# Kernel tuning notes

Measured on AMD Instinct MI355X. Metric: run time of the kernel, lower is better.

The kernel has to match this reference:

```python
import jax, jax.numpy as jnp
import numpy as np

B, T, V, H, F = 128, 20, 10000, 512, 49


def _uniform(key, shape, fan):
    s = 1.0 / np.sqrt(fan)
    return jax.random.uniform(key, shape, jnp.float32, -s, s)


def setup_inputs() -> dict:
    key = jax.random.key(0)
    ks = jax.random.split(key, 16)
    return {
        "caption_inputs": jax.random.randint(ks[0], (B, T), 0, V),
        "global_features": jax.random.normal(ks[1], (B, H), jnp.float32),
        "area_features": jax.random.normal(ks[2], (B, H, F), jnp.float32),
        "h0": jnp.zeros((B, H), jnp.float32),
        "c0": jnp.zeros((B, H), jnp.float32),
        # learned params
        "embedding": jax.random.normal(ks[3], (V, H), jnp.float32),
        "W_ih": _uniform(ks[4], (2 * H, 4 * H), H),   # LSTMCell input weights (x @ W_ih)
        "W_hh": _uniform(ks[5], (H, 4 * H), H),
        "b_ih": _uniform(ks[6], (4 * H,), H),
        "b_hh": _uniform(ks[7], (4 * H,), H),
        "Wv": _uniform(ks[8], (H, H), H),             # attention comp_visual
        "Wh": _uniform(ks[9], (H, H), H),             # attention comp_hidden
        "wo": _uniform(ks[10], (H,), H),              # attention output_layer
        "W_out": _uniform(ks[11], (2 * H, V), 2 * H), # decoder output layer
        "b_out": _uniform(ks[12], (V,), 2 * H),
    }


def reference(caption_inputs, global_features, area_features, h0, c0,
              embedding, W_ih, W_hh, b_ih, b_hh, Wv, Wh, wo, W_out, b_out):
    # Precompute attention visual projection (time-invariant): [B,F,H]
    feat = jnp.swapaxes(area_features, 1, 2)          # [B,F,H]
    Vproj = jnp.einsum('bfh,hk->bfk', feat, Wv)       # [B,F,H]
    bias = b_ih + b_hh

    def step(carry, tok):
        h, c = carry
        emb = embedding[tok]                           # [B,H]
        x = jnp.concatenate([emb, global_features], axis=1)   # [B,2H]
        gates = x @ W_ih + h @ W_hh + bias             # [B,4H]
        i, f, g, o = jnp.split(gates, 4, axis=1)
        c = jax.nn.sigmoid(f) * c + jax.nn.sigmoid(i) * jnp.tanh(g)
        h = jax.nn.sigmoid(o) * jnp.tanh(c)
        # spatial attention over F locations
        z = jnp.tanh(Vproj + (h @ Wh)[:, None, :])     # [B,F,H]
        scores = jnp.einsum('bfh,h->bf', z, wo)        # [B,F]
        alpha = jax.nn.softmax(scores, axis=1)
        attended = jnp.einsum('bhf,bf->bh', area_features, alpha)  # [B,H]
        out = jnp.concatenate([h, attended], axis=1) @ W_out + b_out  # [B,V]
        return (h, c), out

    (_, _), outs = jax.lax.scan(step, (h0, c0), caption_inputs.T)  # [T,B,V]
    return jnp.swapaxes(outs, 0, 1)                    # [B,T,V]
```

## Files before the change

### kernel.cpp

```cpp
#include <hip/hip_runtime.h>

#define B_ 128
#define T_ 20
#define V_ 10000
#define H_ 512
#define F_ 49
#define NBLK_ 128

typedef unsigned short u16;
typedef __attribute__((ext_vector_type(8))) short short8;
typedef __attribute__((ext_vector_type(4))) float floatx4;

#define GLOBAL_AS __attribute__((address_space(1)))
#define LDS_AS    __attribute__((address_space(3)))

__device__ inline void load_lds16(const void* g, void* l) {
    __builtin_amdgcn_global_load_lds((const GLOBAL_AS void*)g, (LDS_AS void*)l, 16, 0, 0);
}

__device__ inline u16 f2b(float v) {
    unsigned u = __builtin_bit_cast(unsigned, v);
    unsigned rounding = 0x7FFFu + ((u >> 16) & 1u);
    return (u16)((u + rounding) >> 16);
}
__device__ inline float b2f(u16 h) {
    unsigned u = ((unsigned)h) << 16;
    return __builtin_bit_cast(float, u);
}
__device__ inline float fast_tanh(float x) {
    return 1.f - 2.f / (__expf(2.f * x) + 1.f);
}
__device__ inline float sigm(float x) { return 1.f / (1.f + __expf(-x)); }

__device__ __forceinline__ void tr32(const float* __restrict__ src, u16* __restrict__ dst,
                                     int K, int N, int bx, int by, int tx, int ty,
                                     float (*tl)[33]) {
    int n0 = bx * 32, k0 = by * 32;
    #pragma unroll
    for (int i = 0; i < 32; i += 8) {
        int k = k0 + ty + i, n = n0 + tx;
        tl[ty + i][tx] = (k < K && n < N) ? src[(size_t)k * N + n] : 0.f;
    }
    __syncthreads();
    #pragma unroll
    for (int i = 0; i < 32; i += 8) {
        int n = n0 + ty + i, k = k0 + tx;
        if (n < N && k < K) dst[(size_t)n * K + k] = f2b(tl[tx][ty + i]);
    }
}

__global__ __launch_bounds__(256) void preamble(
        const float* __restrict__ W_ih, const float* __restrict__ W_hh,
        const float* __restrict__ Wv, const float* __restrict__ Wh,
        const float* __restrict__ W_out, const int* __restrict__ cap,
        const float* __restrict__ emb, const float* __restrict__ gf,
        const float* __restrict__ area, const float* __restrict__ h0,
        u16* __restrict__ WihT, u16* __restrict__ WhhT, u16* __restrict__ WvT,
        u16* __restrict__ WhT, u16* __restrict__ WoutT, u16* __restrict__ X,
        u16* __restrict__ feat, u16* __restrict__ Hall, int* __restrict__ bar) {
    __shared__ float tl[32][33];
    const int bid = blockIdx.x, tid = threadIdx.x;
    const int tx = tid & 31, ty = tid >> 5;

    if (bid < 2048) {
        int r = bid;                 tr32(W_ih, WihT, 1024, 2048, r % 64, r / 64, tx, ty, tl);
    } else if (bid < 3072) {
        int r = bid - 2048;          tr32(W_hh, WhhT, 512, 2048, r % 64, r / 64, tx, ty, tl);
    } else if (bid < 3328) {
        int r = bid - 3072;          tr32(Wv, WvT, 512, 512, r % 16, r / 16, tx, ty, tl);
    } else if (bid < 3584) {
        int r = bid - 3328;          tr32(Wh, WhT, 512, 512, r % 16, r / 16, tx, ty, tl);
    } else if (bid < 13600) {
        int r = bid - 3584;          tr32(W_out, WoutT, 1024, 10000, r % 313, r / 313, tx, ty, tl);
    } else if (bid < 16160) {
        int r = bid - 13600;
        int t = r / B_, b = r % B_;
        int tok = cap[b * T_ + t];
        for (int col = tid; col < 2 * H_; col += 256) {
            float v = (col < H_) ? emb[(size_t)tok * H_ + col] : gf[(size_t)b * H_ + (col - H_)];
            X[(size_t)r * (2 * H_) + col] = f2b(v);
        }
    } else if (bid < 20256) {
        int r = bid - 16160;
        int b = r >> 5, t32 = r & 31;
        int fx = t32 & 1, hy = t32 >> 1;
        tr32(area + (size_t)b * H_ * F_, feat + (size_t)b * F_ * H_,
             H_, F_, fx, hy, tx, ty, tl);
    } else {
        int r = bid - 20256;
        int i = r * 256 + tid;
        Hall[i] = f2b(h0[i]);
        if (r == 0) bar[tid] = 0;
    }
}

__device__ inline void grid_sync_mg(int* base, int ep) {
    __syncthreads();
    if (threadIdx.x == 0) {
        int old = __hip_atomic_fetch_add(&base[0], 1, __ATOMIC_ACQ_REL, __HIP_MEMORY_SCOPE_AGENT);
        if (old == ep * 32 - 1)
            __hip_atomic_store(&base[32], ep, __ATOMIC_RELEASE, __HIP_MEMORY_SCOPE_AGENT);
        while (__hip_atomic_load(&base[32], __ATOMIC_RELAXED, __HIP_MEMORY_SCOPE_AGENT) < ep)
            __builtin_amdgcn_s_sleep(2);
        (void)__hip_atomic_load(&base[32], __ATOMIC_ACQUIRE, __HIP_MEMORY_SCOPE_AGENT);
    }
    __syncthreads();
}

__global__ __launch_bounds__(256, 1) void decode_loop(
        const u16* __restrict__ WhhT, const float* __restrict__ Xin,
        const float* __restrict__ c0, u16* __restrict__ Hall,
        int* __restrict__ bar) {

    __shared__ __align__(16) u16 Whs[64 * 512];
    __shared__ __align__(16) u16 hstage[32 * 512];
    __shared__ float gl[4 * 32 * 16];
    __shared__ float csh[32 * 16];

    const int tid = threadIdx.x;
    const int wave = tid >> 6, lane = tid & 63;
    const int lm = lane & 15, q = lane >> 4;
    const int bid = blockIdx.x;
    const int jg = bid >> 2, mg = bid & 3;
    int* mybar = bar + mg * 64;

    const int lb0 = tid >> 4, jj = tid & 15;
    const int lb1 = lb0 + 16;
    const int grow0 = mg * 32 + lb0, grow1 = mg * 32 + lb1;
    const int j = jg * 16 + jj;

    #pragma unroll
    for (int i = 0; i < 16; ++i) {
        int row = i * 4 + wave;
        int g = row >> 4, lr = row & 15;
        int grr = g * H_ + jg * 16 + lr;
        load_lds16(WhhT + (size_t)grr * H_ + (size_t)(lane ^ (row & 7)) * 8,
                   (char*)Whs + row * 1024);
    }
    csh[tid] = c0[(size_t)grow0 * H_ + j];
    csh[tid + 256] = c0[(size_t)grow1 * H_ + j];

    float xf[8];
    {
        const float* x0 = Xin + (size_t)grow0 * (4 * H_);
        const float* x1 = Xin + (size_t)grow1 * (4 * H_);
        xf[0] = x0[j]; xf[1] = x0[H_ + j]; xf[2] = x0[2 * H_ + j]; xf[3] = x0[3 * H_ + j];
        xf[4] = x1[j]; xf[5] = x1[H_ + j]; xf[6] = x1[2 * H_ + j]; xf[7] = x1[3 * H_ + j];
    }

    for (int t = 0; t < T_; ++t) {
        const u16* hprev = Hall + (size_t)t * B_ * H_;
        u16* hnext = Hall + (size_t)(t + 1) * B_ * H_;

        #pragma unroll
        for (int it = 0; it < 8; ++it) {
            int row = it * 4 + wave;
            load_lds16(hprev + (size_t)(mg * 32 + row) * H_ + (size_t)(lane ^ (row & 7)) * 8,
                       (char*)hstage + row * 1024);
        }
        __syncthreads();

        floatx4 acc0 = {0.f, 0.f, 0.f, 0.f}, acc1 = {0.f, 0.f, 0.f, 0.f};
        #pragma unroll
        for (int kt = 0; kt < 16; ++kt) {
            int ch = kt * 4 + q;
            short8 a0 = *(const short8*)&hstage[(lm << 9) + ((ch ^ (lm & 7)) << 3)];
            short8 a1 = *(const short8*)&hstage[((16 + lm) << 9) + ((ch ^ (lm & 7)) << 3)];
            short8 bb = *(const short8*)&Whs[((wave * 16 + lm) << 9) + ((ch ^ (lm & 7)) << 3)];
            acc0 = __builtin_amdgcn_mfma_f32_16x16x32_bf16(a0, bb, acc0, 0, 0, 0);
            acc1 = __builtin_amdgcn_mfma_f32_16x16x32_bf16(a1, bb, acc1, 0, 0, 0);
        }
        #pragma unroll
        for (int r = 0; r < 4; ++r) {
            gl[wave * 512 + (q * 4 + r) * 16 + lm] = acc0[r];
            gl[wave * 512 + (16 + q * 4 + r) * 16 + lm] = acc1[r];
        }
        __syncthreads();

        float xc[8];
        #pragma unroll
        for (int i = 0; i < 8; ++i) xc[i] = xf[i];
        if (t + 1 < T_) {
            const float* x0 = Xin + ((size_t)(t + 1) * B_ + grow0) * (4 * H_);
            const float* x1 = Xin + ((size_t)(t + 1) * B_ + grow1) * (4 * H_);
            xf[0] = x0[j]; xf[1] = x0[H_ + j]; xf[2] = x0[2 * H_ + j]; xf[3] = x0[3 * H_ + j];
            xf[4] = x1[j]; xf[5] = x1[H_ + j]; xf[6] = x1[2 * H_ + j]; xf[7] = x1[3 * H_ + j];
        }

        {
            float gi = gl[0 * 512 + lb0 * 16 + jj] + xc[0];
            float gf = gl[1 * 512 + lb0 * 16 + jj] + xc[1];
            float gg = gl[2 * 512 + lb0 * 16 + jj] + xc[2];
            float go = gl[3 * 512 + lb0 * 16 + jj] + xc[3];
            float cn = sigm(gf) * csh[tid] + sigm(gi) * fast_tanh(gg);
            csh[tid] = cn;
            hnext[(size_t)grow0 * H_ + j] = f2b(sigm(go) * fast_tanh(cn));
        }
        {
            float gi = gl[0 * 512 + lb1 * 16 + jj] + xc[4];
            float gf = gl[1 * 512 + lb1 * 16 + jj] + xc[5];
            float gg = gl[2 * 512 + lb1 * 16 + jj] + xc[6];
            float go = gl[3 * 512 + lb1 * 16 + jj] + xc[7];
            float cn = sigm(gf) * csh[tid + 256] + sigm(gi) * fast_tanh(gg);
            csh[tid + 256] = cn;
            hnext[(size_t)grow1 * H_ + j] = f2b(sigm(go) * fast_tanh(cn));
        }

        if (t + 1 < T_) grid_sync_mg(mybar, t + 1);
    }
}

__global__ __launch_bounds__(256) void attn_post(
        const float* __restrict__ ahbuf, const u16* __restrict__ Vprojb,
        const u16* __restrict__ feat, const float* __restrict__ wo,
        const u16* __restrict__ Hall, u16* __restrict__ Hcat) {
    __shared__ __align__(16) u16 Vsh[F_ * H_];
    __shared__ __align__(16) u16 fsh[F_ * H_];
    __shared__ float ash[H_];
    __shared__ float wosh[H_];
    __shared__ float sc[64];

    const int tid = threadIdx.x;
    const int wave = tid >> 6, lane = tid & 63;
    const int b = blockIdx.x >> 1, th = blockIdx.x & 1;

    const short8* vsrc = (const short8*)(Vprojb + (size_t)b * F_ * H_);
    const short8* fsrc = (const short8*)(feat + (size_t)b * F_ * H_);
    for (int i = tid; i < F_ * H_ / 8; i += 256) {
        ((short8*)Vsh)[i] = vsrc[i];
        ((short8*)fsh)[i] = fsrc[i];
    }
    for (int i = tid; i < H_; i += 256) wosh[i] = wo[i];
    __syncthreads();

    for (int t = th * (T_ / 2); t < (th + 1) * (T_ / 2); ++t) {
        for (int i = tid; i < H_; i += 256)
            ash[i] = ahbuf[((size_t)t * B_ + b) * H_ + i];
        __syncthreads();

        for (int f = wave; f < F_; f += 4) {
            short8 vv = *(const short8*)&Vsh[f * H_ + lane * 8];
            float s = 0.f;
            #pragma unroll
            for (int e = 0; e < 8; ++e) {
                int h = lane * 8 + e;
                s += wosh[h] * fast_tanh(b2f((u16)vv[e]) + ash[h]);
            }
            #pragma unroll
            for (int off = 32; off; off >>= 1) s += __shfl_xor(s, off);
            if (lane == 0) sc[f] = s;
        }
        __syncthreads();

        if (tid < 64) {
            float v = (tid < F_) ? sc[tid] : -1e30f;
            float m = v;
            #pragma unroll
            for (int off = 32; off; off >>= 1) m = fmaxf(m, __shfl_xor(m, off));
            float e = (tid < F_) ? __expf(v - m) : 0.f;
            float sum = e;
            #pragma unroll
            for (int off = 32; off; off >>= 1) sum += __shfl_xor(sum, off);
            if (tid < F_) sc[tid] = e / sum;
        }
        __syncthreads();

        const size_t rowo = ((size_t)b * T_ + t) * (2 * H_);
        const short8* hrow = (const short8*)(Hall + ((size_t)(t + 1) * B_ + b) * H_);
        for (int i = tid; i < H_ / 8; i += 256)
            ((short8*)(Hcat + rowo))[i] = hrow[i];
        for (int h = tid; h < H_; h += 256) {
            float acc = 0.f;
            #pragma unroll
            for (int f = 0; f < F_; ++f) acc += b2f(fsh[f * H_ + h]) * sc[f];
            Hcat[rowo + H_ + h] = f2b(acc);
        }
        __syncthreads();
    }
}

template <int WRITE_BF16>
__device__ __forceinline__ void gemm2_body(
        const u16* __restrict__ A, int lda, const u16* __restrict__ Bt, int ldb,
        void* __restrict__ Cout, int ldc, const float* __restrict__ bias1,
        const float* __restrict__ bias2, int M, int N, int K, int bx, int by,
        u16* As, u16* Bs) {
    const int tid = threadIdx.x, wave = tid >> 6, lane = tid & 63;
    const int wr = wave >> 1, wc = wave & 1;
    const int lm = lane & 15, q = lane >> 4;
    const int m0 = bx * 128, n0 = by * 128;

    const int off = wave * 1024 + lane * 16;
    const int r0 = off >> 6;
    const int c0 = (off & 63) >> 1;

    const u16* gA0 = A + (size_t)(m0 + r0) * lda + c0;
    const u16* gA1 = A + (size_t)(m0 + r0 + 64) * lda + c0;
    int nb0 = n0 + r0;      if (nb0 > N - 1) nb0 = N - 1;
    int nb1 = n0 + r0 + 64; if (nb1 > N - 1) nb1 = N - 1;
    const u16* gB0 = Bt + (size_t)nb0 * ldb + c0;
    const u16* gB1 = Bt + (size_t)nb1 * ldb + c0;

    floatx4 acc[4][4];
    #pragma unroll
    for (int i = 0; i < 4; ++i)
        #pragma unroll
        for (int jq = 0; jq < 4; ++jq) acc[i][jq] = floatx4{0.f, 0.f, 0.f, 0.f};

    const int nkt = K >> 5;
    {
        load_lds16(gA0, (char*)As + wave * 1024);
        load_lds16(gA1, (char*)As + 4096 + wave * 1024);
        load_lds16(gB0, (char*)Bs + wave * 1024);
        load_lds16(gB1, (char*)Bs + 4096 + wave * 1024);
    }
    __syncthreads();

    int cur = 0;
    for (int kt = 0; kt < nkt; ++kt) {
        if (kt + 1 < nkt) {
            const int ko = (kt + 1) * 32;
            char* dA = (char*)(As + (cur ^ 1) * 4096);
            char* dB = (char*)(Bs + (cur ^ 1) * 4096);
            load_lds16(gA0 + ko, dA + wave * 1024);
            load_lds16(gA1 + ko, dA + 4096 + wave * 1024);
            load_lds16(gB0 + ko, dB + wave * 1024);
            load_lds16(gB1 + ko, dB + 4096 + wave * 1024);
        }
        const u16* Ab = As + cur * 4096;
        const u16* Bb = Bs + cur * 4096;
        short8 af[4], bf[4];
        #pragma unroll
        for (int i = 0; i < 4; ++i)
            af[i] = *(const short8*)&Ab[(wr * 64 + i * 16 + lm) * 32 + q * 8];
        #pragma unroll
        for (int jq = 0; jq < 4; ++jq)
            bf[jq] = *(const short8*)&Bb[(wc * 64 + jq * 16 + lm) * 32 + q * 8];
        #pragma unroll
        for (int i = 0; i < 4; ++i)
            #pragma unroll
            for (int jq = 0; jq < 4; ++jq)
                acc[i][jq] = __builtin_amdgcn_mfma_f32_16x16x32_bf16(af[i], bf[jq], acc[i][jq], 0, 0, 0);
        __syncthreads();
        cur ^= 1;
    }

    #pragma unroll
    for (int i = 0; i < 4; ++i) {
        const int row = m0 + wr * 64 + i * 16 + q * 4;
        #pragma unroll
        for (int jq = 0; jq < 4; ++jq) {
            const int col = n0 + wc * 64 + jq * 16 + lm;
            if (col < N) {
                #pragma unroll
                for (int r = 0; r < 4; ++r) {
                    float v = acc[i][jq][r];
                    if (bias1) v += bias1[col];
                    if (bias2) v += bias2[col];
                    if (WRITE_BF16) ((u16*)Cout)[(size_t)(row + r) * ldc + col] = f2b(v);
                    else            ((float*)Cout)[(size_t)(row + r) * ldc + col] = v;
                }
            }
        }
    }
}

template <int WRITE_BF16>
__global__ __launch_bounds__(256) void gemm2(const u16* __restrict__ A, int lda,
                                             const u16* __restrict__ Bt, int ldb,
                                             void* __restrict__ Cout, int ldc,
                                             const float* __restrict__ bias1,
                                             const float* __restrict__ bias2,
                                             int M, int N, int K) {
    __shared__ __align__(16) u16 As[2 * 128 * 32];
    __shared__ __align__(16) u16 Bs[2 * 128 * 32];
    const int nbx = gridDim.x;
    const int nwg = nbx * gridDim.y;
    const int lin = blockIdx.x + blockIdx.y * nbx;
    const int qq = nwg >> 3, rr = nwg & 7;
    const int xcd = lin & 7, idx = lin >> 3;
    const int wg = (xcd < rr ? xcd * (qq + 1) : rr * (qq + 1) + (xcd - rr) * qq) + idx;
    gemm2_body<WRITE_BF16>(A, lda, Bt, ldb, Cout, ldc, bias1, bias2, M, N, K,
                           wg % nbx, wg / nbx, As, Bs);
}

__global__ __launch_bounds__(256) void gemm_pair(
        const u16* __restrict__ X, const u16* __restrict__ WihT,
        float* __restrict__ Xin, const float* __restrict__ b_ih,
        const float* __restrict__ b_hh, const u16* __restrict__ feat,
        const u16* __restrict__ WvT, u16* __restrict__ Vprojb) {
    __shared__ __align__(16) u16 As[2 * 128 * 32];
    __shared__ __align__(16) u16 Bs[2 * 128 * 32];
    int bid = blockIdx.x;
    if (bid < 320) {
        gemm2_body<0>(X, 2 * H_, WihT, 2 * H_, Xin, 4 * H_, b_ih, b_hh,
                      T_ * B_, 4 * H_, 2 * H_, bid % 20, bid / 20, As, Bs);
    } else {
        int r = bid - 320;
        gemm2_body<1>(feat, H_, WvT, H_, Vprojb, H_, nullptr, nullptr,
                      B_ * F_, H_, H_, r % 49, r / 49, As, Bs);
    }
}

extern "C" void kernel_launch(void* const* d_in, const int* in_sizes, int n_in,
                              void* d_out, int out_size, void* d_ws, size_t ws_size,
                              hipStream_t stream) {
    const int*   cap   = (const int*)d_in[0];
    const float* gf    = (const float*)d_in[1];
    const float* area  = (const float*)d_in[2];
    const float* h0    = (const float*)d_in[3];
    const float* c0    = (const float*)d_in[4];
    const float* emb   = (const float*)d_in[5];
    const float* W_ih  = (const float*)d_in[6];
    const float* W_hh  = (const float*)d_in[7];
    const float* b_ih  = (const float*)d_in[8];
    const float* b_hh  = (const float*)d_in[9];
    const float* Wv    = (const float*)d_in[10];
    const float* Wh    = (const float*)d_in[11];
    const float* wo    = (const float*)d_in[12];
    const float* W_out = (const float*)d_in[13];
    const float* b_out = (const float*)d_in[14];
    float* out = (float*)d_out;

    char* p = (char*)d_ws;
    auto alloc = [&](size_t bytes) {
        char* q = p;
        p += (bytes + 255) & ~(size_t)255;
        return q;
    };
    u16*   X      = (u16*)alloc((size_t)T_ * B_ * 2 * H_ * 2);
    u16*   WihT   = (u16*)alloc((size_t)4 * H_ * 2 * H_ * 2);
    u16*   WhhT   = (u16*)alloc((size_t)4 * H_ * H_ * 2);
    u16*   WvT    = (u16*)alloc((size_t)H_ * H_ * 2);
    u16*   WhT    = (u16*)alloc((size_t)H_ * H_ * 2);
    u16*   WoutT  = (u16*)alloc((size_t)V_ * 2 * H_ * 2);
    u16*   feat   = (u16*)alloc((size_t)B_ * F_ * H_ * 2);
    float* Xin    = (float*)alloc((size_t)T_ * B_ * 4 * H_ * 4);
    u16*   Vprojb = (u16*)alloc((size_t)B_ * F_ * H_ * 2);
    float* ahbuf  = (float*)alloc((size_t)T_ * B_ * H_ * 4);
    u16*   Hall   = (u16*)alloc((size_t)(T_ + 1) * B_ * H_ * 2);
    int*   bar    = (int*)alloc(1024);
    u16*   Hcat   = (u16*)alloc((size_t)B_ * T_ * 2 * H_ * 2);

    preamble<<<20512, 256, 0, stream>>>(W_ih, W_hh, Wv, Wh, W_out, cap, emb, gf,
                                        area, h0, WihT, WhhT, WvT, WhT, WoutT,
                                        X, feat, Hall, bar);

    gemm_pair<<<516, 256, 0, stream>>>(X, WihT, Xin, b_ih, b_hh, feat, WvT, Vprojb);

    decode_loop<<<NBLK_, 256, 0, stream>>>(WhhT, Xin, c0, Hall, bar);

    gemm2<0><<<dim3(T_ * B_ / 128, H_ / 128), 256, 0, stream>>>(
        Hall + (size_t)B_ * H_, H_, WhT, H_, ahbuf, H_, nullptr, nullptr, T_ * B_, H_, H_);

    attn_post<<<2 * B_, 256, 0, stream>>>(ahbuf, Vprojb, feat, wo, Hall, Hcat);

    gemm2<0><<<dim3(T_ * B_ / 128, (V_ + 127) / 128), 256, 0, stream>>>(
        Hcat, 2 * H_, WoutT, 2 * H_, out, V_, b_out, nullptr, T_ * B_, V_, 2 * H_);
}
```

Before: 587.3 us.

## Repartition LSTM decode into 8x16 blocks and replace counter barrier with per-block flags

The recurrent decode loop now assigns each block 16 batch rows and 32 hidden columns instead of 32 rows and 16 columns. This doubles the W_hh slice held in LDS per block and halves the h staging per step. The shared atomic-counter grid barrier is replaced by per-block release flags: one wave polls the 16 flags of its batch group with a wave-wide any(), which removes serialized fetch-add contention on one counter. The element-wise gate update now handles two columns per thread with vectorized loads and a packed bf16 store. The risk is that a larger LDS footprint and more flag polling traffic may offset the gains.

```diff
diff --git a/kernel.cpp b/kernel.cpp
--- a/kernel.cpp
+++ b/kernel.cpp
@@ -10,6 +10,7 @@
 typedef unsigned short u16;
 typedef __attribute__((ext_vector_type(8))) short short8;
 typedef __attribute__((ext_vector_type(4))) float floatx4;
+typedef __attribute__((ext_vector_type(2))) float floatx2;
 
 #define GLOBAL_AS __attribute__((address_space(1)))
 #define LDS_AS    __attribute__((address_space(3)))
@@ -90,21 +91,8 @@
         int r = bid - 20256;
         int i = r * 256 + tid;
         Hall[i] = f2b(h0[i]);
-        if (r == 0) bar[tid] = 0;
-    }
-}
-
-__device__ inline void grid_sync_mg(int* base, int ep) {
-    __syncthreads();
-    if (threadIdx.x == 0) {
-        int old = __hip_atomic_fetch_add(&base[0], 1, __ATOMIC_ACQ_REL, __HIP_MEMORY_SCOPE_AGENT);
-        if (old == ep * 32 - 1)
-            __hip_atomic_store(&base[32], ep, __ATOMIC_RELEASE, __HIP_MEMORY_SCOPE_AGENT);
-        while (__hip_atomic_load(&base[32], __ATOMIC_RELAXED, __HIP_MEMORY_SCOPE_AGENT) < ep)
-            __builtin_amdgcn_s_sleep(2);
-        (void)__hip_atomic_load(&base[32], __ATOMIC_ACQUIRE, __HIP_MEMORY_SCOPE_AGENT);
-    }
-    __syncthreads();
+        if (r < 8) bar[r * 256 + tid] = 0;
+    }
 }
 
 __global__ __launch_bounds__(256, 1) void decode_loop(
@@ -112,40 +100,37 @@
         const float* __restrict__ c0, u16* __restrict__ Hall,
         int* __restrict__ bar) {
 
-    __shared__ __align__(16) u16 Whs[64 * 512];
-    __shared__ __align__(16) u16 hstage[32 * 512];
-    __shared__ float gl[4 * 32 * 16];
-    __shared__ float csh[32 * 16];
+    __shared__ __align__(16) u16 Whs[128 * 512];
+    __shared__ __align__(16) u16 hstage[16 * 512];
+    __shared__ float gl[4 * 16 * 32];
+    __shared__ float csh[16 * 32];
 
     const int tid = threadIdx.x;
     const int wave = tid >> 6, lane = tid & 63;
     const int lm = lane & 15, q = lane >> 4;
     const int bid = blockIdx.x;
-    const int jg = bid >> 2, mg = bid & 3;
-    int* mybar = bar + mg * 64;
-
-    const int lb0 = tid >> 4, jj = tid & 15;
-    const int lb1 = lb0 + 16;
-    const int grow0 = mg * 32 + lb0, grow1 = mg * 32 + lb1;
-    const int j = jg * 16 + jj;
+    const int mg = bid & 7, jg = bid >> 3;
+
+    const int row = tid >> 4, jj = (tid & 15) * 2;
+    const int grow = mg * 16 + row;
+    const int j = jg * 32 + jj;
 
     #pragma unroll
-    for (int i = 0; i < 16; ++i) {
-        int row = i * 4 + wave;
-        int g = row >> 4, lr = row & 15;
-        int grr = g * H_ + jg * 16 + lr;
-        load_lds16(WhhT + (size_t)grr * H_ + (size_t)(lane ^ (row & 7)) * 8,
-                   (char*)Whs + row * 1024);
-    }
-    csh[tid] = c0[(size_t)grow0 * H_ + j];
-    csh[tid + 256] = c0[(size_t)grow1 * H_ + j];
-
-    float xf[8];
+    for (int i = 0; i < 32; ++i) {
+        int r = i * 4 + wave;
+        int g = r >> 5, jr = r & 31;
+        int wrow = g * H_ + jg * 32 + jr;
+        load_lds16(WhhT + (size_t)wrow * H_ + (size_t)(lane ^ (r & 7)) * 8,
+                   (char*)Whs + r * 1024);
+    }
+    csh[row * 32 + jj]     = c0[(size_t)grow * H_ + j];
+    csh[row * 32 + jj + 1] = c0[(size_t)grow * H_ + j + 1];
+
+    floatx2 xf[4];
     {
-        const float* x0 = Xin + (size_t)grow0 * (4 * H_);
-        const float* x1 = Xin + (size_t)grow1 * (4 * H_);
-        xf[0] = x0[j]; xf[1] = x0[H_ + j]; xf[2] = x0[2 * H_ + j]; xf[3] = x0[3 * H_ + j];
-        xf[4] = x1[j]; xf[5] = x1[H_ + j]; xf[6] = x1[2 * H_ + j]; xf[7] = x1[3 * H_ + j];
+        const float* xb = Xin + (size_t)grow * (4 * H_) + j;
+        #pragma unroll
+        for (int g = 0; g < 4; ++g) xf[g] = *(const floatx2*)(xb + g * H_);
     }
 
     for (int t = 0; t < T_; ++t) {
@@ -153,10 +138,10 @@
         u16* hnext = Hall + (size_t)(t + 1) * B_ * H_;
 
         #pragma unroll
-        for (int it = 0; it < 8; ++it) {
-            int row = it * 4 + wave;
-            load_lds16(hprev + (size_t)(mg * 32 + row) * H_ + (size_t)(lane ^ (row & 7)) * 8,
-                       (char*)hstage + row * 1024);
+        for (int i = 0; i < 4; ++i) {
+            int r = i * 4 + wave;
+            load_lds16(hprev + (size_t)(mg * 16 + r) * H_ + (size_t)(lane ^ (r & 7)) * 8,
+                       (char*)hstage + r * 1024);
         }
         __syncthreads();
 
@@ -164,49 +149,70 @@
         #pragma unroll
         for (int kt = 0; kt < 16; ++kt) {
             int ch = kt * 4 + q;
-            short8 a0 = *(const short8*)&hstage[(lm << 9) + ((ch ^ (lm & 7)) << 3)];
-            short8 a1 = *(const short8*)&hstage[((16 + lm) << 9) + ((ch ^ (lm & 7)) << 3)];
-            short8 bb = *(const short8*)&Whs[((wave * 16 + lm) << 9) + ((ch ^ (lm & 7)) << 3)];
-            acc0 = __builtin_amdgcn_mfma_f32_16x16x32_bf16(a0, bb, acc0, 0, 0, 0);
-            acc1 = __builtin_amdgcn_mfma_f32_16x16x32_bf16(a1, bb, acc1, 0, 0, 0);
+            int sw = (ch ^ (lm & 7)) << 3;
+            short8 a  = *(const short8*)&hstage[(lm << 9) + sw];
+            short8 b0 = *(const short8*)&Whs[((wave * 32 + lm) << 9) + sw];
+            short8 b1 = *(const short8*)&Whs[((wave * 32 + 16 + lm) << 9) + sw];
+            acc0 = __builtin_amdgcn_mfma_f32_16x16x32_bf16(a, b0, acc0, 0, 0, 0);
+            acc1 = __builtin_amdgcn_mfma_f32_16x16x32_bf16(a, b1, acc1, 0, 0, 0);
         }
         #pragma unroll
         for (int r = 0; r < 4; ++r) {
-            gl[wave * 512 + (q * 4 + r) * 16 + lm] = acc0[r];
-            gl[wave * 512 + (16 + q * 4 + r) * 16 + lm] = acc1[r];
-        }
-        __syncthreads();
-
-        float xc[8];
-        #pragma unroll
-        for (int i = 0; i < 8; ++i) xc[i] = xf[i];
+            gl[wave * 512 + (q * 4 + r) * 32 + lm]      = acc0[r];
+            gl[wave * 512 + (q * 4 + r) * 32 + 16 + lm] = acc1[r];
+        }
+        __syncthreads();
+
+        floatx2 xc[4];
+        #pragma unroll
+        for (int g = 0; g < 4; ++g) xc[g] = xf[g];
         if (t + 1 < T_) {
-            const float* x0 = Xin + ((size_t)(t + 1) * B_ + grow0) * (4 * H_);
-            const float* x1 = Xin + ((size_t)(t + 1) * B_ + grow1) * (4 * H_);
-            xf[0] = x0[j]; xf[1] = x0[H_ + j]; xf[2] = x0[2 * H_ + j]; xf[3] = x0[3 * H_ + j];
-            xf[4] = x1[j]; xf[5] = x1[H_ + j]; xf[6] = x1[2 * H_ + j]; xf[7] = x1[3 * H_ + j];
+            const float* xb = Xin + ((size_t)(t + 1) * B_ + grow) * (4 * H_) + j;
+            #pragma unroll
+            for (int g = 0; g < 4; ++g) xf[g] = *(const floatx2*)(xb + g * H_);
         }
 
         {
-            float gi = gl[0 * 512 + lb0 * 16 + jj] + xc[0];
-            float gf = gl[1 * 512 + lb0 * 16 + jj] + xc[1];
-            float gg = gl[2 * 512 + lb0 * 16 + jj] + xc[2];
-            float go = gl[3 * 512 + lb0 * 16 + jj] + xc[3];
-            float cn = sigm(gf) * csh[tid] + sigm(gi) * fast_tanh(gg);
-            csh[tid] = cn;
-            hnext[(size_t)grow0 * H_ + j] = f2b(sigm(go) * fast_tanh(cn));
-        }
-        {
-            float gi = gl[0 * 512 + lb1 * 16 + jj] + xc[4];
-            float gf = gl[1 * 512 + lb1 * 16 + jj] + xc[5];
-            float gg = gl[2 * 512 + lb1 * 16 + jj] + xc[6];
-            float go = gl[3 * 512 + lb1 * 16 + jj] + xc[7];
-            float cn = sigm(gf) * csh[tid + 256] + sigm(gi) * fast_tanh(gg);
-            csh[tid + 256] = cn;
-            hnext[(size_t)grow1 * H_ + j] = f2b(sigm(go) * fast_tanh(cn));
-        }
-
-        if (t + 1 < T_) grid_sync_mg(mybar, t + 1);
+            float gi0 = gl[0 * 512 + row * 32 + jj]     + xc[0][0];
+            float gi1 = gl[0 * 512 + row * 32 + jj + 1] + xc[0][1];
+            float gf0 = gl[1 * 512 + row * 32 + jj]     + xc[1][0];
+            float gf1 = gl[1 * 512 + row * 32 + jj + 1] + xc[1][1];
+            float gg0 = gl[2 * 512 + row * 32 + jj]     + xc[2][0];
+            float gg1 = gl[2 * 512 + row * 32 + jj + 1] + xc[2][1];
+            float go0 = gl[3 * 512 + row * 32 + jj]     + xc[3][0];
+            float go1 = gl[3 * 512 + row * 32 + jj + 1] + xc[3][1];
+            float c0n = sigm(gf0) * csh[row * 32 + jj]     + sigm(gi0) * fast_tanh(gg0);
+            float c1n = sigm(gf1) * csh[row * 32 + jj + 1] + sigm(gi1) * fast_tanh(gg1);
+            csh[row * 32 + jj]     = c0n;
+            csh[row * 32 + jj + 1] = c1n;
+            unsigned hv = (unsigned)f2b(sigm(go0) * fast_tanh(c0n)) |
+                          ((unsigned)f2b(sigm(go1) * fast_tanh(c1n)) << 16);
+            *(unsigned*)(hnext + (size_t)grow * H_ + j) = hv;
+        }
+
+        if (t + 1 < T_) {
+            __syncthreads();
+            if (tid == 0)
+                __hip_atomic_store(&bar[(mg * 16 + jg) * 16], t + 1,
+                                   __ATOMIC_RELEASE, __HIP_MEMORY_SCOPE_AGENT);
+            if (wave == 0) {
+                int fl = (lane < 16)
+                    ? __hip_atomic_load(&bar[(mg * 16 + lane) * 16],
+                                        __ATOMIC_RELAXED, __HIP_MEMORY_SCOPE_AGENT)
+                    : (t + 1);
+                while (__any(fl < t + 1)) {
+                    __builtin_amdgcn_s_sleep(1);
+                    fl = (lane < 16)
+                        ? __hip_atomic_load(&bar[(mg * 16 + lane) * 16],
+                                            __ATOMIC_RELAXED, __HIP_MEMORY_SCOPE_AGENT)
+                        : (t + 1);
+                }
+                if (lane == 0)
+                    (void)__hip_atomic_load(&bar[(mg * 16) * 16],
+                                            __ATOMIC_ACQUIRE, __HIP_MEMORY_SCOPE_AGENT);
+            }
+            __syncthreads();
+        }
     }
 }
 
@@ -439,7 +445,7 @@
     u16*   Vprojb = (u16*)alloc((size_t)B_ * F_ * H_ * 2);
     float* ahbuf  = (float*)alloc((size_t)T_ * B_ * H_ * 4);
     u16*   Hall   = (u16*)alloc((size_t)(T_ + 1) * B_ * H_ * 2);
-    int*   bar    = (int*)alloc(1024);
+    int*   bar    = (int*)alloc(8192);
     u16*   Hcat   = (u16*)alloc((size_t)B_ * T_ * 2 * H_ * 2);
 
     preamble<<<20512, 256, 0, stream>>>(W_ih, W_hh, Wv, Wh, W_out, cap, emb, gf,
```

Measured after the change: 569.2 us. 3.1% less time.
